# Kernel optimization log

Measured on AMD Instinct MI355X. Metric: run time of the kernel, lower is better.

Reference implementation:

```python
import jax, jax.numpy as jnp
import numpy as np

D_MODEL = 192
NODE_NUM = 64
DEPTH = 2
ALPHA = 0.05
NUM_LAYERS = 2
LN_EPS = 1e-5


def _gcn(x, p):
    # x: [N, in_dim*D_MODEL]; faithful port of GCN.forward (eval mode)
    nv1, nv2, ws, bs, wm, bm, we, be, wl, bl, g, b = p
    N = x.shape[0]
    in_dim = x.shape[1] // D_MODEL
    adp = jax.nn.softmax(jax.nn.relu(nv1 @ nv2), axis=1)            # [V,V]
    adj = adp + jnp.eye(NODE_NUM, dtype=x.dtype)
    a = adj / adj.sum(1, keepdims=True)                              # row-normalized
    h0 = jax.lax.conv_general_dilated(
        x.reshape(N, in_dim, D_MODEL), ws, (1,), 'VALID',
        dimension_numbers=('NCH', 'OIH', 'NCH')) + bs[None, :, None]  # [N,C,V]
    h = h0
    outs = [h0]
    for _ in range(DEPTH):
        h = ALPHA * h0 + (1.0 - ALPHA) * jnp.einsum('ncw,vw->ncv', h, a)
        outs.append(h)
    ho = jnp.concatenate(outs, axis=1)                               # [N,(DEPTH+1)C,V]
    ho = jax.nn.gelu(jnp.einsum('ncv,oc->nov', ho, wm) + bm[None, :, None], approximate=False)
    ho = jnp.einsum('ncv,oc->nov', ho, we) + be[None, :, None]       # [N,6,V]
    ho = jnp.einsum('nov,dv->nod', ho, wl) + bl                      # [N,6,D]
    mu = ho.mean(-1, keepdims=True)
    var = ((ho - mu) ** 2).mean(-1, keepdims=True)                   # biased, like torch LN
    ho = (ho - mu) / jnp.sqrt(var + LN_EPS) * g + b
    return ho.reshape(N, 6 * D_MODEL)


def _encoder(inp4, flag, layer_params):
    x = jnp.transpose(inp4, (2, 0, 1, 3)) if flag == 1 else jnp.transpose(inp4, (1, 0, 2, 3))
    W, B, O, D = x.shape
    L = W + O - 1
    N = W * B
    # input_transfer: shift row r by r along the slice axis
    place = jax.vmap(lambda xr, r: jax.lax.dynamic_update_slice(
        jnp.zeros((B, L, D), x.dtype), xr, (0, r, 0)))
    a = place(x, jnp.arange(W)).reshape(N, L, D)
    layer0_output = None
    output_all = None
    rows_layers, cols_layers = [], []
    for layer in range(NUM_LAYERS):
        if layer >= 1:
            a = output_all  # eval mode: F.dropout is identity
            if layer == 1:
                layer0_output = a
        p = layer_params[layer]

        def step(carry, x_t, p=p):
            h_row, h_col = carry
            gate = _gcn(jnp.concatenate([h_row, h_col, x_t], axis=-1), p)  # [N,6D]
            sg = jax.nn.sigmoid(gate[:, :4 * D])
            tg = jnp.tanh(gate[:, 4 * D:])
            ug_r, og_r, ug_c, og_c = jnp.split(sg, 4, axis=-1)
            ig_r, ig_c = jnp.split(tg, 2, axis=-1)
            h_row = jnp.tanh((1.0 - ug_r) * h_row + ug_r * ig_r) * og_r
            h_col = jnp.tanh((1.0 - ug_c) * h_col + ug_c * ig_c) * og_c
            out_s = jnp.concatenate([h_row, h_col], axis=-1)
            # col hidden is saved pre-roll, rolled for next step
            return (h_row, jnp.roll(h_col, B, axis=0)), (out_s, h_row, h_col)

        init = (jnp.zeros((N, D), x.dtype), jnp.zeros((N, D), x.dtype))
        _, (outs, hrows, hcols) = jax.lax.scan(step, init, jnp.swapaxes(a, 0, 1))
        output_all = jnp.swapaxes(outs, 0, 1)                        # [N,L,2D]
        if layer >= 1:
            output_all = output_all + layer0_output
        # rows saved at slice s>=O-1 from block loc = s-O+1
        rows = hrows.reshape(L, W, B, D)[jnp.arange(O - 1, L), jnp.arange(W)]  # [W,B,D]
        # cols saved at slice s>=W-1 from last batch block
        cols = hcols[W - 1:, (W - 1) * B:, :]                        # [O,B,D]
        rows_layers.append(rows)
        cols_layers.append(cols)
    hidden_row_all = jnp.stack(rows_layers).transpose(2, 0, 1, 3)    # [B,layers,W,D]
    hidden_col_all = jnp.stack(cols_layers).transpose(2, 0, 1, 3)    # [B,layers,O,D]
    if flag == 1:
        return output_all, hidden_col_all, hidden_row_all
    return output_all, hidden_row_all, hidden_col_all


def setup_inputs() -> dict:
    key = jax.random.key(0)
    ks = jax.random.split(key, 20)
    idx = [0]
    def nxt():
        k = ks[idx[0]]
        idx[0] += 1
        return k
    B, W, O = 8, 24, 48
    K = D_MODEL - NODE_NUM + 1  # 129
    cc, sc, nd = 16, 32, 40
    d = {"input": jax.random.normal(nxt(), (B, W, O, D_MODEL), dtype=jnp.float32)}
    for li, in_dim in enumerate([3, 4]):
        d[f"nodevec1_{li}"] = jax.random.normal(nxt(), (NODE_NUM, nd), dtype=jnp.float32)
        d[f"nodevec2_{li}"] = jax.random.normal(nxt(), (nd, NODE_NUM), dtype=jnp.float32)
        d[f"w_start_{li}"] = jax.random.normal(nxt(), (cc, in_dim, K), dtype=jnp.float32) * 0.05
        d[f"b_start_{li}"] = jnp.zeros((cc,), jnp.float32)
        d[f"w_mlp_{li}"] = jax.random.normal(nxt(), (sc, (DEPTH + 1) * cc), dtype=jnp.float32) * 0.05
        d[f"b_mlp_{li}"] = jnp.zeros((sc,), jnp.float32)
        d[f"w_end_{li}"] = jax.random.normal(nxt(), (6, sc), dtype=jnp.float32) * 0.05
        d[f"b_end_{li}"] = jnp.zeros((6,), jnp.float32)
        d[f"w_lin_{li}"] = jax.random.normal(nxt(), (D_MODEL, NODE_NUM), dtype=jnp.float32) * 0.05
        d[f"b_lin_{li}"] = jnp.zeros((D_MODEL,), jnp.float32)
        d[f"gamma_{li}"] = jnp.ones((D_MODEL,), jnp.float32)
        d[f"beta_{li}"] = jnp.zeros((D_MODEL,), jnp.float32)
    d["flag"] = 0
    return d


def reference(input, nodevec1_0, nodevec2_0, w_start_0, b_start_0, w_mlp_0, b_mlp_0,
              w_end_0, b_end_0, w_lin_0, b_lin_0, gamma_0, beta_0,
              nodevec1_1, nodevec2_1, w_start_1, b_start_1, w_mlp_1, b_mlp_1,
              w_end_1, b_end_1, w_lin_1, b_lin_1, gamma_1, beta_1, flag):
    p0 = (nodevec1_0, nodevec2_0, w_start_0, b_start_0, w_mlp_0, b_mlp_0,
          w_end_0, b_end_0, w_lin_0, b_lin_0, gamma_0, beta_0)
    p1 = (nodevec1_1, nodevec2_1, w_start_1, b_start_1, w_mlp_1, b_mlp_1,
          w_end_1, b_end_1, w_lin_1, b_lin_1, gamma_1, beta_1)
    return _encoder(input, flag, (p0, p1))
```

## Files before the change

kernel.cpp:

```cpp
#include <hip/hip_runtime.h>
#include <hip/hip_bf16.h>

#define NT 1024
typedef unsigned short u16;
typedef unsigned long long u64;

__device__ __forceinline__ u16 tobf(float x) {
  union { __hip_bfloat16 h; u16 u; } cv;
  cv.h = __float2bfloat16(x);
  return cv.u;
}
__device__ __forceinline__ float frombf(u16 u) {
  return __uint_as_float(((unsigned)u) << 16);
}
__device__ __forceinline__ float sigf(float x) {
  return __builtin_amdgcn_rcpf(1.f + __builtin_amdgcn_exp2f(-1.4426950408889634f * x));
}
__device__ __forceinline__ float tanh_fast(float x) {
  return 1.f - 2.f * __builtin_amdgcn_rcpf(1.f + __builtin_amdgcn_exp2f(2.8853900817779268f * x));
}
__device__ __forceinline__ void lds_fence() {
  asm volatile("s_waitcnt lgkmcnt(0)" ::: "memory");
  __builtin_amdgcn_sched_barrier(0);
}
__device__ __forceinline__ void bar_light() {
  asm volatile("s_waitcnt lgkmcnt(0)" ::: "memory");
  __builtin_amdgcn_s_barrier();
  asm volatile("" ::: "memory");
}

struct SeqArgs {
  const float* input;
  const float* nv1_0; const float* nv2_0; const float* nv1_1; const float* nv2_1;
  const float* w_start0; const float* b_start0; const float* w_mlp0; const float* b_mlp0;
  const float* w_end0;   const float* b_end0;   const float* w_lin0; const float* b_lin0;
  const float* gamma0;   const float* beta0;
  const float* w_start1; const float* b_start1; const float* w_mlp1; const float* b_mlp1;
  const float* w_end1;   const float* b_end1;   const float* w_lin1; const float* b_lin1;
  const float* gamma1;   const float* beta1;
  u64*   HCOL2;
  int*   prog;
  float* out_all; float* out_hrow; float* out_hcol;
};

__global__ __launch_bounds__(NT, 4) void seq_kernel(SeqArgs A) {
  const int n = blockIdx.x, w = n >> 3, b = n & 7, tid = threadIdx.x;
  const int pred = (n + 184) % 192;
  const int succ = (n + 8) % 192;

  __shared__ __align__(16) float sCIN[1152];
  __shared__ __align__(16) u16   sWS[64 * 132];
  __shared__ __align__(16) float sAT[4096];
  __shared__ __align__(16) float sH[2][1024];
  __shared__ __align__(16) float sAbuf[4928];
  float* const sPart = sAbuf;
  float* const sG    = sAbuf;
  float* const sH2c  = sAbuf + 2048;
  float* const sE    = sAbuf + 2048;
  float* const sY    = sAbuf;
  float* const smWE  = sAbuf + 3072;
  float* const smBE  = sAbuf + 3264;
  float* const smWM  = sAbuf + 3328;

  for (int layer = 0; layer < 2; ++layer) {
    const int in_dim = 3 + layer;
    const int P = in_dim - 1;
    const float* nv1    = layer ? A.nv1_1    : A.nv1_0;
    const float* nv2    = layer ? A.nv2_1    : A.nv2_0;
    const float* wstart = layer ? A.w_start1 : A.w_start0;
    const float* bs     = layer ? A.b_start1 : A.b_start0;
    const float* wm     = layer ? A.w_mlp1   : A.w_mlp0;
    const float* bm     = layer ? A.b_mlp1   : A.b_mlp0;
    const float* we     = layer ? A.w_end1   : A.w_end0;
    const float* be     = layer ? A.b_end1   : A.b_end0;
    const float* wl     = layer ? A.w_lin1   : A.w_lin0;
    const float* bl     = layer ? A.b_lin1   : A.b_lin0;
    const float* gm     = layer ? A.gamma1   : A.gamma0;
    const float* bt     = layer ? A.beta1    : A.beta0;

    for (int idx = tid; idx < 4096; idx += NT) {
      int v = idx >> 6, ww = idx & 63;
      float s = 0.f;
      for (int j = 0; j < 40; ++j) s = fmaf(nv1[v*40 + j], nv2[j*64 + ww], s);
      sAbuf[idx] = fmaxf(s, 0.f);
    }
    __syncthreads();
    if (tid < 64) {
      const int v = tid;
      float m = -1e30f;
      for (int ww = 0; ww < 64; ++ww) m = fmaxf(m, sAbuf[v*64 + ww]);
      float s = 0.f;
      for (int ww = 0; ww < 64; ++ww) { float e = expf(sAbuf[v*64 + ww] - m); sAbuf[v*64 + ww] = e; s += e; }
      float inv = 1.f / s, rs = 1.f;
      for (int ww = 0; ww < 64; ++ww) rs += sAbuf[v*64 + ww] * inv;
      float irs = 1.f / rs;
      for (int ww = 0; ww < 64; ++ww) {
        float a = sAbuf[v*64 + ww] * inv + ((ww == v) ? 1.f : 0.f);
        sAT[ww*64 + v] = a * irs;
      }
    }
    __syncthreads();
    for (int idx = tid; idx < 16*in_dim*132; idx += NT) {
      int row = idx / 132, k = idx - row*132;
      sWS[idx] = (k < 129) ? tobf(wstart[((row & 15)*in_dim + (row >> 4))*129 + k]) : (u16)0;
    }
    for (int idx = tid; idx < 1536; idx += NT) { int o = idx/48, c = idx - o*48; smWM[o*50 + c] = wm[idx]; }
    for (int idx = tid; idx < 192; idx += NT) smWE[idx] = we[idx];
    if (tid < 6) smBE[tid] = be[tid];
    for (int d = tid; d < 384; d += NT) sCIN[d] = 0.f;

    const int v_p = tid & 63;
    const int o0  = tid >> 6;
    const float bmv0 = bm[o0], bmv1 = bm[o0 + 16];
    float blv = 0.f, gmv = 1.f, btv = 0.f;
    if (tid < 384) blv = bl[(tid >= 192) ? tid - 192 : tid];
    if (tid < 192) { gmv = gm[tid]; btv = bt[tid]; }
    const float bs_r0 = bs[o0];
    __syncthreads();

    auto pre_conv = [&](int parity) {
      const float* xb = &sCIN[384 + parity*384];
      const int nslots = P << 9;
      for (int s = tid; s < nslots; s += NT) {
        const int cidx = s >> 5;
        const int vg2  = s & 31;
        const int p = cidx >> 4, c = cidx & 15;
        const int ich = (p == 0) ? 0 : (p + 1);
        const float* xin = ((p == 0) ? &sCIN[0] : &xb[(p-1)*192]) + vg2*2;
        const u16* wrow = &sWS[(ich*16 + c)*132];
        float a0 = 0.f, a1 = 0.f;
        float2 xc = *(const float2*)xin;
        for (int k2 = 0; k2 < 128; k2 += 2) {
          ushort2 wu = *(const ushort2*)(wrow + k2);
          float w0 = frombf(wu.x), w1 = frombf(wu.y);
          float2 xn = *(const float2*)(xin + k2 + 2);
          a0 = fmaf(w1, xc.y, fmaf(w0, xc.x, a0));
          a1 = fmaf(w1, xn.x, fmaf(w0, xc.y, a1));
          xc = xn;
        }
        float wk = frombf(wrow[128]);
        a0 = fmaf(wk, xc.x, a0); a1 = fmaf(wk, xc.y, a1);
        *(float2*)&sPart[cidx*64 + vg2*2] = make_float2(a0, a1);
      }
      bar_light();
      {
        const int c0 = o0, v = v_p;
        float sum = bs_r0;
        for (int p = 0; p < P; ++p) sum += sPart[(p*16 + c0)*64 + v];
        sH[0][c0*64 + v] = sum;
      }
      bar_light();
    };

    {
      float* xb = &sCIN[384];
      if (layer == 0) {
        int o = 0 - w;
        if (o >= 0 && o < 48) {
          const float* xr = A.input + (((size_t)(b*24 + w)*48 + o)*192);
          for (int d = tid; d < 192; d += NT) xb[d] = xr[d];
        } else {
          for (int d = tid; d < 192; d += NT) xb[d] = 0.f;
        }
      } else {
        const float* xr = A.out_all + ((size_t)n*71 + 0)*384;
        for (int d = tid; d < 384; d += NT) xb[d] = xr[d];
      }
      bar_light();
      pre_conv(0);
    }

    for (int t = 0; t < 71; ++t) {
      const int S = layer*71 + t;

      if (t > 0) {
        if (tid < 192) {
          const u64* src = &A.HCOL2[((size_t)((S-1) & 15)*192 + pred)*192 + tid];
          u64 v = __hip_atomic_load(src, __ATOMIC_RELAXED, __HIP_MEMORY_SCOPE_AGENT);
          while ((unsigned)(v >> 32) != (unsigned)S) {
            __builtin_amdgcn_s_sleep(1);
            v = __hip_atomic_load(src, __ATOMIC_RELAXED, __HIP_MEMORY_SCOPE_AGENT);
          }
          __builtin_amdgcn_sched_barrier(0);
          asm volatile("" ::: "memory");
          sCIN[192 + tid] = __uint_as_float((unsigned)v);
        }
        bar_light();
        if (tid == 0)
          __hip_atomic_store(&A.prog[n*32], S, __ATOMIC_RELAXED, __HIP_MEMORY_SCOPE_AGENT);
      }

      if (tid < 512) {
        {
          const int c = tid >> 5, vg2 = tid & 31;
          const int vbase = c*64 + vg2*2;
          const float* xin = &sCIN[192 + vg2*2];
          const u16* wrow = &sWS[(16 + c)*132];
          float a0 = sH[0][vbase], a1 = sH[0][vbase + 1];
          float2 xc = *(const float2*)xin;
          for (int k2 = 0; k2 < 128; k2 += 2) {
            ushort2 wu = *(const ushort2*)(wrow + k2);
            float w0 = frombf(wu.x), w1 = frombf(wu.y);
            float2 xn = *(const float2*)(xin + k2 + 2);
            a0 = fmaf(w1, xc.y, fmaf(w0, xc.x, a0));
            a1 = fmaf(w1, xn.x, fmaf(w0, xc.y, a1));
            xc = xn;
          }
          float wk = frombf(wrow[128]);
          a0 = fmaf(wk, xc.x, a0); a1 = fmaf(wk, xc.y, a1);
          sH[0][vbase] = a0; sH[0][vbase + 1] = a1;
        }
        lds_fence();
        {
          const int c0 = o0 * 2;
          float pa0 = 0.f, pa1 = 0.f;
          for (int w4 = 0; w4 < 64; w4 += 4) {
            float a0v = sAT[(w4+0)*64 + v_p];
            float a1v = sAT[(w4+1)*64 + v_p];
            float a2v = sAT[(w4+2)*64 + v_p];
            float a3v = sAT[(w4+3)*64 + v_p];
            float4 h0v = *(const float4*)&sH[0][ c0      *64 + w4];
            float4 h1v = *(const float4*)&sH[0][(c0 + 1 )*64 + w4];
            pa0 = fmaf(h0v.x, a0v, pa0); pa0 = fmaf(h0v.y, a1v, pa0);
            pa0 = fmaf(h0v.z, a2v, pa0); pa0 = fmaf(h0v.w, a3v, pa0);
            pa1 = fmaf(h1v.x, a0v, pa1); pa1 = fmaf(h1v.y, a1v, pa1);
            pa1 = fmaf(h1v.z, a2v, pa1); pa1 = fmaf(h1v.w, a3v, pa1);
          }
          float h0a = sH[0][ c0      *64 + v_p];
          float h0b = sH[0][(c0 + 1 )*64 + v_p];
          sH[1][ c0      *64 + v_p] = fmaf(0.95f, pa0, 0.05f * h0a);
          sH[1][(c0 + 1 )*64 + v_p] = fmaf(0.95f, pa1, 0.05f * h0b);
          lds_fence();
          float pb0 = 0.f, pb1 = 0.f;
          for (int w4 = 0; w4 < 64; w4 += 4) {
            float a0v = sAT[(w4+0)*64 + v_p];
            float a1v = sAT[(w4+1)*64 + v_p];
            float a2v = sAT[(w4+2)*64 + v_p];
            float a3v = sAT[(w4+3)*64 + v_p];
            float4 h0v = *(const float4*)&sH[1][ c0      *64 + w4];
            float4 h1v = *(const float4*)&sH[1][(c0 + 1 )*64 + w4];
            pb0 = fmaf(h0v.x, a0v, pb0); pb0 = fmaf(h0v.y, a1v, pb0);
            pb0 = fmaf(h0v.z, a2v, pb0); pb0 = fmaf(h0v.w, a3v, pb0);
            pb1 = fmaf(h1v.x, a0v, pb1); pb1 = fmaf(h1v.y, a1v, pb1);
            pb1 = fmaf(h1v.z, a2v, pb1); pb1 = fmaf(h1v.w, a3v, pb1);
          }
          sH2c[ c0      *64 + v_p] = fmaf(0.95f, pb0, 0.05f * h0a);
          sH2c[(c0 + 1 )*64 + v_p] = fmaf(0.95f, pb1, 0.05f * h0b);
        }
      } else {
        if (t < 70) {
          const int d = tid - 512;
          float* xb = &sCIN[384 + ((t+1) & 1)*384];
          if (layer == 0) {
            if (d < 192) {
              int o = (t + 1) - w;
              xb[d] = (o >= 0 && o < 48)
                    ? A.input[(((size_t)(b*24 + w)*48 + o)*192) + d] : 0.f;
            }
          } else {
            if (d < 384) xb[d] = A.out_all[((size_t)n*71 + (t+1))*384 + d];
          }
        }
        if (tid == 960 && S >= 16) {
          while (__hip_atomic_load(&A.prog[succ*32], __ATOMIC_RELAXED, __HIP_MEMORY_SCOPE_AGENT) < S - 15)
            __builtin_amdgcn_s_sleep(2);
        }
      }
      bar_light();

      {
        float g0 = bmv0, g1 = bmv1;
#pragma unroll
        for (int c = 0; c < 16; ++c) {
          float h0v = sH[0][c*64 + v_p];
          float h1v = sH[1][c*64 + v_p];
          float h2v = sH2c[c*64 + v_p];
          g0 = fmaf(smWM[ o0      *50 + c], h0v, fmaf(smWM[ o0      *50 + 16 + c], h1v, fmaf(smWM[ o0      *50 + 32 + c], h2v, g0)));
          g1 = fmaf(smWM[(o0+16 )*50 + c], h0v, fmaf(smWM[(o0+16 )*50 + 16 + c], h1v, fmaf(smWM[(o0+16 )*50 + 32 + c], h2v, g1)));
        }
        g0 = 0.5f * g0 * (1.f + erff(g0 * 0.70710678118654752f));
        g1 = 0.5f * g1 * (1.f + erff(g1 * 0.70710678118654752f));
        sG[ o0      *64 + v_p] = g0;
        sG[(o0+16 )*64 + v_p] = g1;
      }
      bar_light();

      for (int idx = tid; idx < 384; idx += NT) {
        int o2 = idx >> 6, v = idx & 63;
        float acc = smBE[o2];
        for (int c = 0; c < 32; ++c) acc = fmaf(smWE[o2*32 + c], sG[c*64 + v], acc);
        sE[idx] = acc;
      }
      bar_light();

      if (tid < 384) {
        const int d  = (tid >= 192) ? tid - 192 : tid;
        const int r0 = (tid >= 192) ? 3 : 0;
        const float4* wrow = (const float4*)(wl + d*64);
        float y0 = blv, y1 = blv, y2 = blv;
        for (int q = 0; q < 16; ++q) {
          float4 wv = wrow[q];
          float4 e0 = *(const float4*)&sE[(r0+0)*64 + q*4];
          float4 e1 = *(const float4*)&sE[(r0+1)*64 + q*4];
          float4 e2 = *(const float4*)&sE[(r0+2)*64 + q*4];
          y0 = fmaf(e0.x,wv.x, fmaf(e0.y,wv.y, fmaf(e0.z,wv.z, fmaf(e0.w,wv.w, y0))));
          y1 = fmaf(e1.x,wv.x, fmaf(e1.y,wv.y, fmaf(e1.z,wv.z, fmaf(e1.w,wv.w, y1))));
          y2 = fmaf(e2.x,wv.x, fmaf(e2.y,wv.y, fmaf(e2.z,wv.z, fmaf(e2.w,wv.w, y2))));
        }
        sY[(r0+0)*192 + d] = y0;
        sY[(r0+1)*192 + d] = y1;
        sY[(r0+2)*192 + d] = y2;
      }
      bar_light();

      if (tid < 192) {
        const int r = tid >> 5, l32 = tid & 31;
        float sm = 0.f, sq = 0.f;
#pragma unroll
        for (int m = 0; m < 6; ++m) {
          float v = sY[r*192 + l32 + 32*m];
          sm += v; sq = fmaf(v, v, sq);
        }
#pragma unroll
        for (int off = 16; off >= 1; off >>= 1) {
          sm += __shfl_xor(sm, off);
          sq += __shfl_xor(sq, off);
        }
        if (l32 == 0) {
          float mu = sm * (1.f/192.f);
          float var = sq * (1.f/192.f) - mu*mu;
          sH[1][r] = mu;
          sH[1][8 + r] = rsqrtf(fmaxf(var, 0.f) + 1e-5f);
        }
      }
      bar_light();

      float hcn = 0.f;
      if (tid < 192) {
        const int d = tid;
        float y2 = fmaf((sY[2*192+d] - sH[1][2]) * sH[1][10], gmv, btv);
        float y3 = fmaf((sY[3*192+d] - sH[1][3]) * sH[1][11], gmv, btv);
        float y5 = fmaf((sY[5*192+d] - sH[1][5]) * sH[1][13], gmv, btv);
        float ugc = sigf(y2), ogc = sigf(y3), igc = tanh_fast(y5);
        float hc = sCIN[192 + d];
        hcn = tanh_fast(fmaf(ugc, igc, (1.f - ugc)*hc)) * ogc;
        u64 pk = ((u64)(unsigned)(S + 1) << 32) | (u64)__float_as_uint(hcn);
        __hip_atomic_store(&A.HCOL2[((size_t)(S & 15)*192 + n)*192 + d], pk,
                           __ATOMIC_RELAXED, __HIP_MEMORY_SCOPE_AGENT);
      }
      if (tid < 192) {
        const int d = tid;
        float y0 = fmaf((sY[0*192+d] - sH[1][0]) * sH[1][8],  gmv, btv);
        float y1 = fmaf((sY[1*192+d] - sH[1][1]) * sH[1][9],  gmv, btv);
        float y4 = fmaf((sY[4*192+d] - sH[1][4]) * sH[1][12], gmv, btv);
        float ugr = sigf(y0), ogr = sigf(y1), igr = tanh_fast(y4);
        float hr = sCIN[d];
        float hrn = tanh_fast(fmaf(ugr, igr, (1.f - ugr)*hr)) * ogr;
        sCIN[d] = hrn;
        float* oa = A.out_all + ((size_t)n*71 + t)*384;
        if (layer == 0) { oa[d] = hrn; oa[192 + d] = hcn; }
        else {
          const float* xbt = &sCIN[384 + (t & 1)*384];
          oa[d] = hrn + xbt[d]; oa[192 + d] = hcn + xbt[192 + d];
        }
        if (t == 47 + w)
          A.out_hrow[(((size_t)b*2 + layer)*24 + w)*192 + d] = hrn;
        if (w == 23 && t >= 23)
          A.out_hcol[(((size_t)b*2 + layer)*48 + (t - 23))*192 + d] = hcn;
      }
      bar_light();
      if (t < 70) pre_conv((t + 1) & 1);
    }
    __syncthreads();
  }
}

extern "C" void kernel_launch(void* const* d_in, const int* in_sizes, int n_in,
                              void* d_out, int out_size, void* d_ws, size_t ws_size,
                              hipStream_t stream) {
  (void)in_sizes; (void)n_in; (void)out_size; (void)ws_size;
  char* ws = (char*)d_ws;
  int* prog  = (int*)ws;
  u64* HCOL2 = (u64*)(ws + 24576);

  hipMemsetAsync(ws, 0, 24576 + 4718592, stream);

  SeqArgs A;
  A.input    = (const float*)d_in[0];
  A.nv1_0    = (const float*)d_in[1];  A.nv2_0 = (const float*)d_in[2];
  A.w_start0 = (const float*)d_in[3];  A.b_start0 = (const float*)d_in[4];
  A.w_mlp0   = (const float*)d_in[5];  A.b_mlp0   = (const float*)d_in[6];
  A.w_end0   = (const float*)d_in[7];  A.b_end0   = (const float*)d_in[8];
  A.w_lin0   = (const float*)d_in[9];  A.b_lin0   = (const float*)d_in[10];
  A.gamma0   = (const float*)d_in[11]; A.beta0    = (const float*)d_in[12];
  A.nv1_1    = (const float*)d_in[13]; A.nv2_1 = (const float*)d_in[14];
  A.w_start1 = (const float*)d_in[15]; A.b_start1 = (const float*)d_in[16];
  A.w_mlp1   = (const float*)d_in[17]; A.b_mlp1   = (const float*)d_in[18];
  A.w_end1   = (const float*)d_in[19]; A.b_end1   = (const float*)d_in[20];
  A.w_lin1   = (const float*)d_in[21]; A.b_lin1   = (const float*)d_in[22];
  A.gamma1   = (const float*)d_in[23]; A.beta1    = (const float*)d_in[24];
  A.HCOL2 = HCOL2; A.prog = prog;
  A.out_all  = (float*)d_out;
  A.out_hrow = (float*)d_out + 5234688;
  A.out_hcol = (float*)d_out + 5308416;

  seq_kernel<<<192, NT, 0, stream>>>(A);
}
```

Before: 2.674 ms.

## Overlap next-step input convolution with gating and widen conv to four outputs

The start-conv over the input channels for step t+1 now runs on idle threads (tid>=512) while the end-projection runs, so only the h_row channel convolution stays serialized after the LSTM update. The conv inner loop now computes four adjacent outputs per thread using float4 loads, and the diffusion matmuls give each thread four rows instead of two. Shared buffers are split apart so regions no longer alias, and the row/col gate updates move to separate thread groups. This adds LDS usage and more work per thread in the serial critical path, which could lower occupancy.

```diff
diff --git a/kernel.cpp b/kernel.cpp
--- a/kernel.cpp
+++ b/kernel.cpp
@@ -27,6 +27,25 @@
   asm volatile("s_waitcnt lgkmcnt(0)" ::: "memory");
   __builtin_amdgcn_s_barrier();
   asm volatile("" ::: "memory");
+}
+
+__device__ __forceinline__ void conv4(const u16* __restrict__ wrow,
+                                      const float* __restrict__ xin,
+                                      float& a0, float& a1, float& a2, float& a3) {
+  float4 xc = *(const float4*)xin;
+  for (int k4 = 0; k4 < 128; k4 += 4) {
+    ushort4 wu = *(const ushort4*)(wrow + k4);
+    float w0 = frombf(wu.x), w1 = frombf(wu.y), w2 = frombf(wu.z), w3 = frombf(wu.w);
+    float4 xn = *(const float4*)(xin + k4 + 4);
+    a0 = fmaf(w3, xc.w, fmaf(w2, xc.z, fmaf(w1, xc.y, fmaf(w0, xc.x, a0))));
+    a1 = fmaf(w3, xn.x, fmaf(w2, xc.w, fmaf(w1, xc.z, fmaf(w0, xc.y, a1))));
+    a2 = fmaf(w3, xn.y, fmaf(w2, xn.x, fmaf(w1, xc.w, fmaf(w0, xc.z, a2))));
+    a3 = fmaf(w3, xn.z, fmaf(w2, xn.y, fmaf(w1, xn.x, fmaf(w0, xc.w, a3))));
+    xc = xn;
+  }
+  float wk = frombf(wrow[128]);
+  a0 = fmaf(wk, xc.x, a0); a1 = fmaf(wk, xc.y, a1);
+  a2 = fmaf(wk, xc.z, a2); a3 = fmaf(wk, xc.w, a3);
 }
 
 struct SeqArgs {
@@ -48,19 +67,21 @@
   const int pred = (n + 184) % 192;
   const int succ = (n + 8) % 192;
 
-  __shared__ __align__(16) float sCIN[1152];
-  __shared__ __align__(16) u16   sWS[64 * 132];
-  __shared__ __align__(16) float sAT[4096];
-  __shared__ __align__(16) float sH[2][1024];
-  __shared__ __align__(16) float sAbuf[4928];
+  __shared__ __align__(16) float  sCIN[1152];
+  __shared__ __align__(16) u16    sWS[64 * 132];
+  __shared__ __align__(16) float  sAT[4096];
+  __shared__ __align__(16) float  sH0[1024];
+  __shared__ __align__(16) float  sH1[1024];
+  __shared__ __align__(16) float2 hI2[1024];
+  __shared__ __align__(16) float  sAbuf[4096];
+  __shared__ __align__(16) float  sG[2048];
+  __shared__ __align__(16) float  sY[1152];
+  __shared__ __align__(16) float  smWE[192];
+  __shared__ __align__(16) float  smBE[8];
+  __shared__ __align__(16) float  smWM[32 * 52];
   float* const sPart = sAbuf;
-  float* const sG    = sAbuf;
-  float* const sH2c  = sAbuf + 2048;
-  float* const sE    = sAbuf + 2048;
-  float* const sY    = sAbuf;
-  float* const smWE  = sAbuf + 3072;
-  float* const smBE  = sAbuf + 3264;
-  float* const smWM  = sAbuf + 3328;
+  float* const sE    = sAbuf + 3072;
+  float* const smSt  = sAbuf + 3456;
 
   for (int layer = 0; layer < 2; ++layer) {
     const int in_dim = 3 + layer;
@@ -104,7 +125,7 @@
       int row = idx / 132, k = idx - row*132;
       sWS[idx] = (k < 129) ? tobf(wstart[((row & 15)*in_dim + (row >> 4))*129 + k]) : (u16)0;
     }
-    for (int idx = tid; idx < 1536; idx += NT) { int o = idx/48, c = idx - o*48; smWM[o*50 + c] = wm[idx]; }
+    for (int idx = tid; idx < 1536; idx += NT) { int o = idx/48, c = idx - o*48; smWM[o*52 + c] = wm[idx]; }
     for (int idx = tid; idx < 192; idx += NT) smWE[idx] = we[idx];
     if (tid < 6) smBE[tid] = be[tid];
     for (int d = tid; d < 384; d += NT) sCIN[d] = 0.f;
@@ -112,62 +133,41 @@
     const int v_p = tid & 63;
     const int o0  = tid >> 6;
     const float bmv0 = bm[o0], bmv1 = bm[o0 + 16];
-    float blv = 0.f, gmv = 1.f, btv = 0.f;
+    const float bs_r0 = bs[o0];
+    float blv = 0.f;
     if (tid < 384) blv = bl[(tid >= 192) ? tid - 192 : tid];
-    if (tid < 192) { gmv = gm[tid]; btv = bt[tid]; }
-    const float bs_r0 = bs[o0];
+    const int dg = (tid < 192) ? tid : ((tid >= 256 && tid < 448) ? tid - 256 : 0);
+    const float gmv = gm[dg], btv = bt[dg];
     __syncthreads();
 
-    auto pre_conv = [&](int parity) {
-      const float* xb = &sCIN[384 + parity*384];
-      const int nslots = P << 9;
-      for (int s = tid; s < nslots; s += NT) {
-        const int cidx = s >> 5;
-        const int vg2  = s & 31;
-        const int p = cidx >> 4, c = cidx & 15;
-        const int ich = (p == 0) ? 0 : (p + 1);
-        const float* xin = ((p == 0) ? &sCIN[0] : &xb[(p-1)*192]) + vg2*2;
-        const u16* wrow = &sWS[(ich*16 + c)*132];
-        float a0 = 0.f, a1 = 0.f;
-        float2 xc = *(const float2*)xin;
-        for (int k2 = 0; k2 < 128; k2 += 2) {
-          ushort2 wu = *(const ushort2*)(wrow + k2);
-          float w0 = frombf(wu.x), w1 = frombf(wu.y);
-          float2 xn = *(const float2*)(xin + k2 + 2);
-          a0 = fmaf(w1, xc.y, fmaf(w0, xc.x, a0));
-          a1 = fmaf(w1, xn.x, fmaf(w0, xc.y, a1));
-          xc = xn;
-        }
-        float wk = frombf(wrow[128]);
-        a0 = fmaf(wk, xc.x, a0); a1 = fmaf(wk, xc.y, a1);
-        *(float2*)&sPart[cidx*64 + vg2*2] = make_float2(a0, a1);
-      }
-      bar_light();
-      {
-        const int c0 = o0, v = v_p;
-        float sum = bs_r0;
-        for (int p = 0; p < P; ++p) sum += sPart[(p*16 + c0)*64 + v];
-        sH[0][c0*64 + v] = sum;
-      }
-      bar_light();
-    };
-
     {
-      float* xb = &sCIN[384];
+      float* xb0 = &sCIN[384];
       if (layer == 0) {
         int o = 0 - w;
-        if (o >= 0 && o < 48) {
-          const float* xr = A.input + (((size_t)(b*24 + w)*48 + o)*192);
-          for (int d = tid; d < 192; d += NT) xb[d] = xr[d];
-        } else {
-          for (int d = tid; d < 192; d += NT) xb[d] = 0.f;
-        }
+        for (int d = tid; d < 192; d += NT)
+          xb0[d] = (o >= 0 && o < 48) ? A.input[(((size_t)(b*24 + w)*48 + o)*192) + d] : 0.f;
       } else {
-        const float* xr = A.out_all + ((size_t)n*71 + 0)*384;
-        for (int d = tid; d < 384; d += NT) xb[d] = xr[d];
-      }
-      bar_light();
-      pre_conv(0);
+        for (int d = tid; d < 384; d += NT)
+          xb0[d] = A.out_all[((size_t)n*71 + 0)*384 + d];
+      }
+      bar_light();
+      const int nps = P << 8;
+      if (tid < nps) {
+        int p = tid >> 8, c = (tid >> 4) & 15, v0 = (tid & 15) * 4;
+        int ich = (p == 0) ? 0 : (p + 1);
+        const float* xin = ((p == 0) ? &sCIN[0] : &xb0[(p-1)*192]) + v0;
+        float a0 = 0.f, a1 = 0.f, a2 = 0.f, a3 = 0.f;
+        conv4(&sWS[(ich*16 + c)*132], xin, a0, a1, a2, a3);
+        *(float4*)&sPart[(p*16 + c)*64 + v0] = make_float4(a0, a1, a2, a3);
+      }
+      bar_light();
+      {
+        int c = tid >> 6, v = tid & 63;
+        float sum = bs_r0;
+        for (int p = 0; p < P; ++p) sum += sPart[(p*16 + c)*64 + v];
+        sH0[c*64 + v] = sum;
+      }
+      bar_light();
     }
 
     for (int t = 0; t < 71; ++t) {
@@ -190,106 +190,123 @@
           __hip_atomic_store(&A.prog[n*32], S, __ATOMIC_RELAXED, __HIP_MEMORY_SCOPE_AGENT);
       }
 
-      if (tid < 512) {
+      if (tid < 256) {
+        const int c  = tid >> 4, v0 = (tid & 15) * 4;
         {
-          const int c = tid >> 5, vg2 = tid & 31;
-          const int vbase = c*64 + vg2*2;
-          const float* xin = &sCIN[192 + vg2*2];
-          const u16* wrow = &sWS[(16 + c)*132];
-          float a0 = sH[0][vbase], a1 = sH[0][vbase + 1];
-          float2 xc = *(const float2*)xin;
-          for (int k2 = 0; k2 < 128; k2 += 2) {
-            ushort2 wu = *(const ushort2*)(wrow + k2);
-            float w0 = frombf(wu.x), w1 = frombf(wu.y);
-            float2 xn = *(const float2*)(xin + k2 + 2);
-            a0 = fmaf(w1, xc.y, fmaf(w0, xc.x, a0));
-            a1 = fmaf(w1, xn.x, fmaf(w0, xc.y, a1));
-            xc = xn;
+          float4 acc = *(const float4*)&sH0[c*64 + v0];
+          float a0 = acc.x, a1 = acc.y, a2 = acc.z, a3 = acc.w;
+          conv4(&sWS[(16 + c)*132], &sCIN[192 + v0], a0, a1, a2, a3);
+          *(float4*)&sH0[c*64 + v0] = make_float4(a0, a1, a2, a3);
+        }
+        lds_fence();
+        const int r0 = (tid >> 6) * 4;
+        float h0a[4];
+#pragma unroll
+        for (int j = 0; j < 4; ++j) h0a[j] = sH0[(r0+j)*64 + v_p];
+        float pa[4] = {0.f, 0.f, 0.f, 0.f};
+        for (int w4 = 0; w4 < 64; w4 += 4) {
+          float a0v = sAT[(w4+0)*64 + v_p];
+          float a1v = sAT[(w4+1)*64 + v_p];
+          float a2v = sAT[(w4+2)*64 + v_p];
+          float a3v = sAT[(w4+3)*64 + v_p];
+#pragma unroll
+          for (int j = 0; j < 4; ++j) {
+            float4 hv = *(const float4*)&sH0[(r0+j)*64 + w4];
+            pa[j] = fmaf(hv.x, a0v, pa[j]); pa[j] = fmaf(hv.y, a1v, pa[j]);
+            pa[j] = fmaf(hv.z, a2v, pa[j]); pa[j] = fmaf(hv.w, a3v, pa[j]);
           }
-          float wk = frombf(wrow[128]);
-          a0 = fmaf(wk, xc.x, a0); a1 = fmaf(wk, xc.y, a1);
-          sH[0][vbase] = a0; sH[0][vbase + 1] = a1;
+        }
+#pragma unroll
+        for (int j = 0; j < 4; ++j) {
+          float h1v = fmaf(0.95f, pa[j], 0.05f * h0a[j]);
+          sH1[(r0+j)*64 + v_p] = h1v;
+          hI2[(r0+j)*64 + v_p].x = h1v;
         }
         lds_fence();
-        {
-          const int c0 = o0 * 2;
-          float pa0 = 0.f, pa1 = 0.f;
-          for (int w4 = 0; w4 < 64; w4 += 4) {
-            float a0v = sAT[(w4+0)*64 + v_p];
-            float a1v = sAT[(w4+1)*64 + v_p];
-            float a2v = sAT[(w4+2)*64 + v_p];
-            float a3v = sAT[(w4+3)*64 + v_p];
-            float4 h0v = *(const float4*)&sH[0][ c0      *64 + w4];
-            float4 h1v = *(const float4*)&sH[0][(c0 + 1 )*64 + w4];
-            pa0 = fmaf(h0v.x, a0v, pa0); pa0 = fmaf(h0v.y, a1v, pa0);
-            pa0 = fmaf(h0v.z, a2v, pa0); pa0 = fmaf(h0v.w, a3v, pa0);
-            pa1 = fmaf(h1v.x, a0v, pa1); pa1 = fmaf(h1v.y, a1v, pa1);
-            pa1 = fmaf(h1v.z, a2v, pa1); pa1 = fmaf(h1v.w, a3v, pa1);
+        float pb[4] = {0.f, 0.f, 0.f, 0.f};
+        for (int w4 = 0; w4 < 64; w4 += 4) {
+          float a0v = sAT[(w4+0)*64 + v_p];
+          float a1v = sAT[(w4+1)*64 + v_p];
+          float a2v = sAT[(w4+2)*64 + v_p];
+          float a3v = sAT[(w4+3)*64 + v_p];
+#pragma unroll
+          for (int j = 0; j < 4; ++j) {
+            float4 hv = *(const float4*)&sH1[(r0+j)*64 + w4];
+            pb[j] = fmaf(hv.x, a0v, pb[j]); pb[j] = fmaf(hv.y, a1v, pb[j]);
+            pb[j] = fmaf(hv.z, a2v, pb[j]); pb[j] = fmaf(hv.w, a3v, pb[j]);
           }
-          float h0a = sH[0][ c0      *64 + v_p];
-          float h0b = sH[0][(c0 + 1 )*64 + v_p];
-          sH[1][ c0      *64 + v_p] = fmaf(0.95f, pa0, 0.05f * h0a);
-          sH[1][(c0 + 1 )*64 + v_p] = fmaf(0.95f, pa1, 0.05f * h0b);
-          lds_fence();
-          float pb0 = 0.f, pb1 = 0.f;
-          for (int w4 = 0; w4 < 64; w4 += 4) {
-            float a0v = sAT[(w4+0)*64 + v_p];
-            float a1v = sAT[(w4+1)*64 + v_p];
-            float a2v = sAT[(w4+2)*64 + v_p];
-            float a3v = sAT[(w4+3)*64 + v_p];
-            float4 h0v = *(const float4*)&sH[1][ c0      *64 + w4];
-            float4 h1v = *(const float4*)&sH[1][(c0 + 1 )*64 + w4];
-            pb0 = fmaf(h0v.x, a0v, pb0); pb0 = fmaf(h0v.y, a1v, pb0);
-            pb0 = fmaf(h0v.z, a2v, pb0); pb0 = fmaf(h0v.w, a3v, pb0);
-            pb1 = fmaf(h1v.x, a0v, pb1); pb1 = fmaf(h1v.y, a1v, pb1);
-            pb1 = fmaf(h1v.z, a2v, pb1); pb1 = fmaf(h1v.w, a3v, pb1);
-          }
-          sH2c[ c0      *64 + v_p] = fmaf(0.95f, pb0, 0.05f * h0a);
-          sH2c[(c0 + 1 )*64 + v_p] = fmaf(0.95f, pb1, 0.05f * h0b);
-        }
-      } else {
+        }
+#pragma unroll
+        for (int j = 0; j < 4; ++j)
+          hI2[(r0+j)*64 + v_p].y = fmaf(0.95f, pb[j], 0.05f * h0a[j]);
+      } else if (tid >= 512) {
         if (t < 70) {
           const int d = tid - 512;
-          float* xb = &sCIN[384 + ((t+1) & 1)*384];
+          float* xbn = &sCIN[384 + ((t+1) & 1)*384];
           if (layer == 0) {
             if (d < 192) {
               int o = (t + 1) - w;
-              xb[d] = (o >= 0 && o < 48)
-                    ? A.input[(((size_t)(b*24 + w)*48 + o)*192) + d] : 0.f;
+              xbn[d] = (o >= 0 && o < 48)
+                     ? A.input[(((size_t)(b*24 + w)*48 + o)*192) + d] : 0.f;
             }
           } else {
-            if (d < 384) xb[d] = A.out_all[((size_t)n*71 + (t+1))*384 + d];
+            if (d < 384) xbn[d] = A.out_all[((size_t)n*71 + (t+1))*384 + d];
           }
         }
-        if (tid == 960 && S >= 16) {
-          while (__hip_atomic_load(&A.prog[succ*32], __ATOMIC_RELAXED, __HIP_MEMORY_SCOPE_AGENT) < S - 15)
-            __builtin_amdgcn_s_sleep(2);
-        }
+      } else if (tid == 320 && S >= 16) {
+        while (__hip_atomic_load(&A.prog[succ*32], __ATOMIC_RELAXED, __HIP_MEMORY_SCOPE_AGENT) < S - 15)
+          __builtin_amdgcn_s_sleep(2);
       }
       bar_light();
 
       {
         float g0 = bmv0, g1 = bmv1;
-#pragma unroll
-        for (int c = 0; c < 16; ++c) {
-          float h0v = sH[0][c*64 + v_p];
-          float h1v = sH[1][c*64 + v_p];
-          float h2v = sH2c[c*64 + v_p];
-          g0 = fmaf(smWM[ o0      *50 + c], h0v, fmaf(smWM[ o0      *50 + 16 + c], h1v, fmaf(smWM[ o0      *50 + 32 + c], h2v, g0)));
-          g1 = fmaf(smWM[(o0+16 )*50 + c], h0v, fmaf(smWM[(o0+16 )*50 + 16 + c], h1v, fmaf(smWM[(o0+16 )*50 + 32 + c], h2v, g1)));
+        for (int cq = 0; cq < 4; ++cq) {
+          float4 wa0 = *(const float4*)&smWM[ o0      *52      + cq*4];
+          float4 wb0 = *(const float4*)&smWM[ o0      *52 + 16 + cq*4];
+          float4 wc0 = *(const float4*)&smWM[ o0      *52 + 32 + cq*4];
+          float4 wa1 = *(const float4*)&smWM[(o0 + 16)*52      + cq*4];
+          float4 wb1 = *(const float4*)&smWM[(o0 + 16)*52 + 16 + cq*4];
+          float4 wc1 = *(const float4*)&smWM[(o0 + 16)*52 + 32 + cq*4];
+#pragma unroll
+          for (int j = 0; j < 4; ++j) {
+            int c = cq*4 + j;
+            float h0v = sH0[c*64 + v_p];
+            float2 hh = hI2[c*64 + v_p];
+            g0 = fmaf(((const float*)&wa0)[j], h0v,
+                 fmaf(((const float*)&wb0)[j], hh.x,
+                 fmaf(((const float*)&wc0)[j], hh.y, g0)));
+            g1 = fmaf(((const float*)&wa1)[j], h0v,
+                 fmaf(((const float*)&wb1)[j], hh.x,
+                 fmaf(((const float*)&wc1)[j], hh.y, g1)));
+          }
         }
         g0 = 0.5f * g0 * (1.f + erff(g0 * 0.70710678118654752f));
         g1 = 0.5f * g1 * (1.f + erff(g1 * 0.70710678118654752f));
         sG[ o0      *64 + v_p] = g0;
-        sG[(o0+16 )*64 + v_p] = g1;
-      }
-      bar_light();
-
-      for (int idx = tid; idx < 384; idx += NT) {
-        int o2 = idx >> 6, v = idx & 63;
+        sG[(o0 + 16)*64 + v_p] = g1;
+      }
+      bar_light();
+
+      if (tid < 384) {
+        int o2 = tid >> 6, v = tid & 63;
         float acc = smBE[o2];
-        for (int c = 0; c < 32; ++c) acc = fmaf(smWE[o2*32 + c], sG[c*64 + v], acc);
-        sE[idx] = acc;
+        for (int c4 = 0; c4 < 8; ++c4) {
+          float4 wev = *(const float4*)&smWE[o2*32 + c4*4];
+#pragma unroll
+          for (int j = 0; j < 4; ++j)
+            acc = fmaf(((const float*)&wev)[j], sG[(c4*4+j)*64 + v], acc);
+        }
+        sE[tid] = acc;
+      } else if (tid >= 512 && t < 70) {
+        int s = tid - 512;
+        if (s < ((P-1) << 8)) {
+          int p = 1 + (s >> 8), c = (s >> 4) & 15, v0 = (s & 15) * 4;
+          const float* xin = &sCIN[384 + ((t+1) & 1)*384 + (p-1)*192 + v0];
+          float a0 = 0.f, a1 = 0.f, a2 = 0.f, a3 = 0.f;
+          conv4(&sWS[((p+1)*16 + c)*132], xin, a0, a1, a2, a3);
+          *(float4*)&sPart[(p*16 + c)*64 + v0] = make_float4(a0, a1, a2, a3);
+        }
       }
       bar_light();
 
@@ -329,47 +346,59 @@
         if (l32 == 0) {
           float mu = sm * (1.f/192.f);
           float var = sq * (1.f/192.f) - mu*mu;
-          sH[1][r] = mu;
-          sH[1][8 + r] = rsqrtf(fmaxf(var, 0.f) + 1e-5f);
-        }
-      }
-      bar_light();
-
-      float hcn = 0.f;
+          smSt[r] = mu;
+          smSt[8 + r] = rsqrtf(fmaxf(var, 0.f) + 1e-5f);
+        }
+      }
+      bar_light();
+
       if (tid < 192) {
         const int d = tid;
-        float y2 = fmaf((sY[2*192+d] - sH[1][2]) * sH[1][10], gmv, btv);
-        float y3 = fmaf((sY[3*192+d] - sH[1][3]) * sH[1][11], gmv, btv);
-        float y5 = fmaf((sY[5*192+d] - sH[1][5]) * sH[1][13], gmv, btv);
+        float y2 = fmaf((sY[2*192+d] - smSt[2]) * smSt[10], gmv, btv);
+        float y3 = fmaf((sY[3*192+d] - smSt[3]) * smSt[11], gmv, btv);
+        float y5 = fmaf((sY[5*192+d] - smSt[5]) * smSt[13], gmv, btv);
         float ugc = sigf(y2), ogc = sigf(y3), igc = tanh_fast(y5);
         float hc = sCIN[192 + d];
-        hcn = tanh_fast(fmaf(ugc, igc, (1.f - ugc)*hc)) * ogc;
+        float hcn = tanh_fast(fmaf(ugc, igc, (1.f - ugc)*hc)) * ogc;
         u64 pk = ((u64)(unsigned)(S + 1) << 32) | (u64)__float_as_uint(hcn);
         __hip_atomic_store(&A.HCOL2[((size_t)(S & 15)*192 + n)*192 + d], pk,
                            __ATOMIC_RELAXED, __HIP_MEMORY_SCOPE_AGENT);
-      }
-      if (tid < 192) {
-        const int d = tid;
-        float y0 = fmaf((sY[0*192+d] - sH[1][0]) * sH[1][8],  gmv, btv);
-        float y1 = fmaf((sY[1*192+d] - sH[1][1]) * sH[1][9],  gmv, btv);
-        float y4 = fmaf((sY[4*192+d] - sH[1][4]) * sH[1][12], gmv, btv);
+        float* oa = A.out_all + ((size_t)n*71 + t)*384;
+        oa[192 + d] = layer ? (hcn + sCIN[384 + (t & 1)*384 + 192 + d]) : hcn;
+        if (w == 23 && t >= 23)
+          A.out_hcol[(((size_t)b*2 + layer)*48 + (t - 23))*192 + d] = hcn;
+      } else if (tid >= 256 && tid < 448) {
+        const int d = tid - 256;
+        float y0 = fmaf((sY[0*192+d] - smSt[0]) * smSt[8],  gmv, btv);
+        float y1 = fmaf((sY[1*192+d] - smSt[1]) * smSt[9],  gmv, btv);
+        float y4 = fmaf((sY[4*192+d] - smSt[4]) * smSt[12], gmv, btv);
         float ugr = sigf(y0), ogr = sigf(y1), igr = tanh_fast(y4);
         float hr = sCIN[d];
         float hrn = tanh_fast(fmaf(ugr, igr, (1.f - ugr)*hr)) * ogr;
         sCIN[d] = hrn;
         float* oa = A.out_all + ((size_t)n*71 + t)*384;
-        if (layer == 0) { oa[d] = hrn; oa[192 + d] = hcn; }
-        else {
-          const float* xbt = &sCIN[384 + (t & 1)*384];
-          oa[d] = hrn + xbt[d]; oa[192 + d] = hcn + xbt[192 + d];
-        }
+        oa[d] = layer ? (hrn + sCIN[384 + (t & 1)*384 + d]) : hrn;
         if (t == 47 + w)
           A.out_hrow[(((size_t)b*2 + layer)*24 + w)*192 + d] = hrn;
-        if (w == 23 && t >= 23)
-          A.out_hcol[(((size_t)b*2 + layer)*48 + (t - 23))*192 + d] = hcn;
-      }
-      bar_light();
-      if (t < 70) pre_conv((t + 1) & 1);
+      }
+      bar_light();
+
+      if (t < 70) {
+        if (tid < 256) {
+          int c = tid >> 4, v0 = (tid & 15) * 4;
+          float a0 = 0.f, a1 = 0.f, a2 = 0.f, a3 = 0.f;
+          conv4(&sWS[c*132], &sCIN[v0], a0, a1, a2, a3);
+          *(float4*)&sPart[c*64 + v0] = make_float4(a0, a1, a2, a3);
+        }
+        bar_light();
+        {
+          int c = tid >> 6, v = tid & 63;
+          float sum = bs_r0;
+          for (int p = 0; p < P; ++p) sum += sPart[(p*16 + c)*64 + v];
+          sH0[c*64 + v] = sum;
+        }
+        bar_light();
+      }
     }
     __syncthreads();
   }
@@ -383,7 +412,7 @@
   int* prog  = (int*)ws;
   u64* HCOL2 = (u64*)(ws + 24576);
 
-  hipMemsetAsync(ws, 0, 24576 + 4718592, stream);
+  (void)hipMemsetAsync(ws, 0, 24576 + 4718592, stream);
 
   SeqArgs A;
   A.input    = (const float*)d_in[0];
```

Result: slower. 3.147 ms (+17.7%).
